# Kernel optimization log

Hardware: AMD Instinct MI355X
Metric: run time of the kernel (lower is better)

Reference implementation:

```python
import jax, jax.numpy as jnp
import numpy as np

D_HEAD = 64  # per-head dim 'd' from init_kwargs


def layer_norm(x, g, b, eps=1e-5):
    m = x.mean(-1, keepdims=True)
    v = x.var(-1, keepdims=True)  # biased var, matches torch LayerNorm
    return (x - m) / jnp.sqrt(v + eps) * g + b


def setup_inputs() -> dict:
    key = jax.random.key(0)
    ks = jax.random.split(key, 16)
    F = 512
    B, T, N = 2, 8, 1024
    s = 1.0 / np.sqrt(F)
    u = lambda k, shape: jax.random.uniform(k, shape, jnp.float32, -s, s)
    return {
        "x": jax.random.normal(ks[0], (B, T, N, F), jnp.float32),
        "Wq": u(ks[1], (F, F)), "bq": u(ks[2], (F,)),
        "Wk": u(ks[3], (F, F)), "bk": u(ks[4], (F,)),
        "Wv": u(ks[5], (F, F)), "bv": u(ks[6], (F,)),
        "ln_g": jnp.ones((F,), jnp.float32), "ln_b": jnp.zeros((F,), jnp.float32),
        "W1": u(ks[7], (F, F)), "b1": u(ks[8], (F,)),
        "W2": u(ks[9], (F, F)), "b2": u(ks[10], (F,)),
        "lnff_g": jnp.ones((F,), jnp.float32), "lnff_b": jnp.zeros((F,), jnp.float32),
    }


def reference(x, Wq, bq, Wk, bk, Wv, bv, ln_g, ln_b, W1, b1, W2, b2, lnff_g, lnff_b):
    B, T, N, F = x.shape
    h = F // D_HEAD
    # q/k/v projections
    q = x @ Wq + bq
    k = x @ Wk + bk
    v = x @ Wv + bv
    # split last dim into heads (split+cat(dim=0) in torch == head axis here)
    qh = q.reshape(B, T, N, h, D_HEAD)
    kh = k.reshape(B, T, N, h, D_HEAD)
    vh = v.reshape(B, T, N, h, D_HEAD)
    # attention over node axis N per (batch, time, head)
    A = jnp.einsum('btqhd,btkhd->bthqk', qh, kh) / jnp.sqrt(jnp.asarray(D_HEAD, x.dtype))
    A = jax.nn.softmax(A, axis=-1)
    o = jnp.einsum('bthqk,btkhd->btqhd', A, vh).reshape(B, T, N, F)
    # residual + LN
    val = layer_norm(o + x, ln_g, ln_b)
    # FFN + final LN
    ff = jax.nn.relu(val @ W1 + b1) @ W2 + b2
    return layer_norm(ff, lnff_g, lnff_b)
```

## Files before the change

kernel.cpp:

```cpp
#include <hip/hip_runtime.h>
#include <hip/hip_bf16.h>

using bf16 = __hip_bfloat16;
typedef unsigned int u32x4 __attribute__((ext_vector_type(4)));
typedef float f32x4 __attribute__((ext_vector_type(4)));
typedef __bf16 bf16x8 __attribute__((ext_vector_type(8)));

#define DEVI __device__ __forceinline__

DEVI f32x4 mfma16(u32x4 a, u32x4 b, f32x4 c) {
    return __builtin_amdgcn_mfma_f32_16x16x32_bf16(
        __builtin_bit_cast(bf16x8, a), __builtin_bit_cast(bf16x8, b), c, 0, 0, 0);
}

struct bf8 { bf16 h[8]; };

DEVI u32x4 pack8(f32x4 lo, f32x4 hi) {
    bf8 t;
#pragma unroll
    for (int i = 0; i < 4; i++) {
        t.h[i] = __float2bfloat16(lo[i]);
        t.h[4 + i] = __float2bfloat16(hi[i]);
    }
    return __builtin_bit_cast(u32x4, t);
}

DEVI unsigned long long pk4(float a, float b, float c, float d) {
    union { unsigned long long u; bf16 h[4]; } t;
    t.h[0] = __float2bfloat16(a); t.h[1] = __float2bfloat16(b);
    t.h[2] = __float2bfloat16(c); t.h[3] = __float2bfloat16(d);
    return t.u;
}

DEVI unsigned trunc2(float a, float b) {
    return __builtin_amdgcn_perm(__builtin_bit_cast(unsigned, b),
                                 __builtin_bit_cast(unsigned, a), 0x07060302);
}

__global__ __launch_bounds__(256) void prep(
    const float* __restrict__ Wq, const float* __restrict__ Wk,
    const float* __restrict__ Wv, const float* __restrict__ W1,
    const float* __restrict__ W2, const float* __restrict__ x,
    bf16* __restrict__ WT, bf16* __restrict__ xb)
{
    int b = blockIdx.x;
    if (b < 5120) {
        int w = b >> 10;
        const float* src = (w == 0) ? Wq : (w == 1) ? Wk : (w == 2) ? Wv : (w == 3) ? W1 : W2;
        int idx = (b & 1023) * 256 + threadIdx.x;
        int n = idx >> 9, kk = idx & 511;
        WT[(size_t)w * 262144 + idx] = __float2bfloat16(src[kk * 512 + n]);
    } else {
        size_t i = ((size_t)(b - 5120) * 256 + threadIdx.x) * 8;
        f32x4 lo = *(const f32x4*)&x[i];
        f32x4 hi = *(const f32x4*)&x[i + 4];
        *(u32x4*)&xb[i] = pack8(lo, hi);
    }
}

#define GEMM_BODY(EPILOGUE)                                                          \
    constexpr int SP = 72;                                                           \
    __shared__ __align__(16) bf16 As[128 * SP];                                      \
    __shared__ __align__(16) bf16 Bs[128 * SP];                                      \
    const int tid = threadIdx.x;                                                     \
    const int lane = tid & 63, wave = tid >> 6;                                      \
    const int wm = (wave >> 1) * 64, wn = (wave & 1) * 64;                           \
    const int lm = lane & 15, lq = lane >> 4;                                        \
    const int sr = tid >> 3, sc = (tid & 7) * 8;             \
    const bf16* Ap = A + (size_t)(bm + sr) * 512 + sc;                               \
    const bf16* Bp = Bt + (size_t)(bn + sr) * 512 + sc;                              \
    f32x4 acc[4][4];                                                                 \
    _Pragma("unroll") for (int i = 0; i < 4; i++)                                    \
        _Pragma("unroll") for (int j = 0; j < 4; j++)                                \
            acc[i][j] = (f32x4){0.f, 0.f, 0.f, 0.f};                                 \
    u32x4 ar[4], br[4];                                                              \
    _Pragma("unroll") for (int p = 0; p < 4; p++) {                                  \
        ar[p] = *(const u32x4*)(Ap + (size_t)p * 32 * 512);                          \
        br[p] = *(const u32x4*)(Bp + (size_t)p * 32 * 512);                          \
    }                                                                                \
    for (int k0 = 0; k0 < 512; k0 += 64) {                                           \
        __syncthreads();                                                             \
        _Pragma("unroll") for (int p = 0; p < 4; p++) {                              \
            *(u32x4*)&As[(p * 32 + sr) * SP + sc] = ar[p];                           \
            *(u32x4*)&Bs[(p * 32 + sr) * SP + sc] = br[p];                           \
        }                                                                            \
        __syncthreads();                                                             \
        if (k0 < 448) {      \
            _Pragma("unroll") for (int p = 0; p < 4; p++) {                          \
                ar[p] = *(const u32x4*)(Ap + (size_t)p * 32 * 512 + k0 + 64);        \
                br[p] = *(const u32x4*)(Bp + (size_t)p * 32 * 512 + k0 + 64);        \
            }                                                                        \
        }                                                                            \
        _Pragma("unroll") for (int h = 0; h < 2; h++) {                              \
            u32x4 af[4], bfr[4];                                                     \
            _Pragma("unroll") for (int i = 0; i < 4; i++)                            \
                af[i] = *(const u32x4*)&As[(wm + i * 16 + lm) * SP + h * 32 + lq * 8]; \
            _Pragma("unroll") for (int j = 0; j < 4; j++)                            \
                bfr[j] = *(const u32x4*)&Bs[(wn + j * 16 + lm) * SP + h * 32 + lq * 8]; \
            EPILOGUE##_MMA                                                           \
        }                                                                            \
    }

#define SWAPPED_MMA                                                                  \
    _Pragma("unroll") for (int i = 0; i < 4; i++)                                    \
        _Pragma("unroll") for (int j = 0; j < 4; j++)                                \
            acc[i][j] = mfma16(bfr[j], af[i], acc[i][j]);
#define NORMAL_MMA                                                                   \
    _Pragma("unroll") for (int i = 0; i < 4; i++)                                    \
        _Pragma("unroll") for (int j = 0; j < 4; j++)                                \
            acc[i][j] = mfma16(af[i], bfr[j], acc[i][j]);

__global__ __launch_bounds__(256) void gemm_qkv(
    const bf16* __restrict__ A, const bf16* __restrict__ WT,
    const float* __restrict__ bqp, const float* __restrict__ bkp, const float* __restrict__ bvp,
    bf16* __restrict__ qb, bf16* __restrict__ kb, bf16* __restrict__ vT)
{
    const int wsel = blockIdx.y >> 2;
    const int bm = blockIdx.x * 128, bn = (blockIdx.y & 3) * 128;
    const bf16* Bt = WT + (size_t)wsel * 262144;
    const float* bias = (wsel == 0) ? bqp : (wsel == 1) ? bkp : bvp;

    if (wsel < 2) {
        GEMM_BODY(SWAPPED)
        const float scale = (wsel == 0) ? 0.18033688f : 1.0f;
        bf16* dst = (wsel == 0) ? qb : kb;
#pragma unroll
        for (int i = 0; i < 4; i++) {
#pragma unroll
            for (int j = 0; j < 4; j++) {
                int row = bm + wm + i * 16 + lm;
                int colb = bn + wn + j * 16 + lq * 4;
                f32x4 b4 = *(const f32x4*)&bias[colb];
                *(unsigned long long*)&dst[(size_t)row * 512 + colb] =
                    pk4((acc[i][j][0] + b4[0]) * scale, (acc[i][j][1] + b4[1]) * scale,
                        (acc[i][j][2] + b4[2]) * scale, (acc[i][j][3] + b4[3]) * scale);
            }
        }
    } else {
        GEMM_BODY(NORMAL)
#pragma unroll
        for (int i = 0; i < 4; i++) {
#pragma unroll
            for (int j = 0; j < 4; j++) {
                int col = bn + wn + j * 16 + lm;
                float bv = bias[col];
                int rowb = bm + wm + i * 16 + lq * 4;
                int btq = rowb >> 10, node = rowb & 1023;
                int u = node & 31;
                int nodeP = (node & ~31) | (((u >> 2) & 3) << 3) | (((u >> 4) & 1) << 2);
                *(unsigned long long*)&vT[((size_t)((btq * 8 + (col >> 6)) * 64 + (col & 63))) * 1024 + nodeP] =
                    pk4(acc[i][j][0] + bv, acc[i][j][1] + bv,
                        acc[i][j][2] + bv, acc[i][j][3] + bv);
            }
        }
    }
}

template <bool RELU>
__global__ __launch_bounds__(256) void gemm_bt(
    const bf16* __restrict__ A, const bf16* __restrict__ Bt,
    const float* __restrict__ bias, bf16* __restrict__ C)
{
    const int bm = blockIdx.x * 128, bn = blockIdx.y * 128;
    GEMM_BODY(SWAPPED)
#pragma unroll
    for (int i = 0; i < 4; i++) {
#pragma unroll
        for (int j = 0; j < 4; j++) {
            int row = bm + wm + i * 16 + lm;
            int colb = bn + wn + j * 16 + lq * 4;
            f32x4 b4 = *(const f32x4*)&bias[colb];
            float c0 = acc[i][j][0] + b4[0], c1 = acc[i][j][1] + b4[1];
            float c2 = acc[i][j][2] + b4[2], c3 = acc[i][j][3] + b4[3];
            if (RELU) {
                c0 = fmaxf(c0, 0.f); c1 = fmaxf(c1, 0.f);
                c2 = fmaxf(c2, 0.f); c3 = fmaxf(c3, 0.f);
            }
            *(unsigned long long*)&C[(size_t)row * 512 + colb] = pk4(c0, c1, c2, c3);
        }
    }
}

__global__ __launch_bounds__(256, 4) void attn_kernel(
    const bf16* __restrict__ q, const bf16* __restrict__ k,
    const bf16* __restrict__ vT, float* __restrict__ o)
{
    constexpr int KP = 72;
    constexpr int VP = 72;
    __shared__ __align__(16) bf16 Ks[64 * KP];
    __shared__ __align__(16) bf16 Vs[64 * VP];

    const int tid = threadIdx.x, lane = tid & 63, wave = tid >> 6;
    const int group = blockIdx.x;
    const int bt = group >> 3, hh = group & 7;
    const int lm = lane & 15, lq = lane >> 4;
    const int qrow0 = bt * 1024 + blockIdx.y * 128 + wave * 32;

    u32x4 qf[2][2];
#pragma unroll
    for (int tm = 0; tm < 2; tm++)
#pragma unroll
        for (int kk2 = 0; kk2 < 2; kk2++)
            qf[tm][kk2] = *(const u32x4*)&q[(size_t)(qrow0 + tm * 16 + lm) * 512 + hh * 64 + kk2 * 32 + lq * 8];

    const bf16* kbase = k + (size_t)(bt * 1024) * 512 + hh * 64;
    const bf16* vbase = vT + (size_t)group * 64 * 1024;

    const int r0 = tid >> 3, e0 = (tid & 7) * 8;
    const int r1 = (256 + tid) >> 3, e1 = e0;

    f32x4 accO[4][2];
#pragma unroll
    for (int md = 0; md < 4; md++)
#pragma unroll
        for (int tm = 0; tm < 2; tm++) accO[md][tm] = (f32x4){0.f, 0.f, 0.f, 0.f};
    float part[2] = {0.f, 0.f};

    u32x4 kreg0 = *(const u32x4*)&kbase[(size_t)r0 * 512 + e0];
    u32x4 kreg1 = *(const u32x4*)&kbase[(size_t)r1 * 512 + e1];
    u32x4 vreg0 = *(const u32x4*)&vbase[(size_t)r0 * 1024 + e0];
    u32x4 vreg1 = *(const u32x4*)&vbase[(size_t)r1 * 1024 + e1];

    for (int kt = 0; kt < 16; kt++) {
        __syncthreads();
        *(u32x4*)&Ks[r0 * KP + e0] = kreg0;
        *(u32x4*)&Ks[r1 * KP + e1] = kreg1;
        *(u32x4*)&Vs[r0 * VP + e0] = vreg0;
        *(u32x4*)&Vs[r1 * VP + e1] = vreg1;
        __syncthreads();
        if (kt < 15) {
            const bf16* kn = kbase + (size_t)((kt + 1) * 64) * 512;
            const bf16* vn = vbase + (kt + 1) * 64;
            kreg0 = *(const u32x4*)&kn[(size_t)r0 * 512 + e0];
            kreg1 = *(const u32x4*)&kn[(size_t)r1 * 512 + e1];
            vreg0 = *(const u32x4*)&vn[(size_t)r0 * 1024 + e0];
            vreg1 = *(const u32x4*)&vn[(size_t)r1 * 1024 + e1];
        }

#pragma unroll
        for (int kc = 0; kc < 2; kc++) {
            const int t0 = kc * 2;
            u32x4 kf00 = *(const u32x4*)&Ks[(t0 * 16 + lm) * KP + lq * 8];
            u32x4 kf01 = *(const u32x4*)&Ks[(t0 * 16 + lm) * KP + 32 + lq * 8];
            u32x4 kf10 = *(const u32x4*)&Ks[((t0 + 1) * 16 + lm) * KP + lq * 8];
            u32x4 kf11 = *(const u32x4*)&Ks[((t0 + 1) * 16 + lm) * KP + 32 + lq * 8];
            u32x4 pw[2];
#pragma unroll
            for (int tm = 0; tm < 2; tm++) {
                f32x4 s0 = (f32x4){0.f, 0.f, 0.f, 0.f};
                s0 = mfma16(kf00, qf[tm][0], s0);
                s0 = mfma16(kf01, qf[tm][1], s0);
                f32x4 s1 = (f32x4){0.f, 0.f, 0.f, 0.f};
                s1 = mfma16(kf10, qf[tm][0], s1);
                s1 = mfma16(kf11, qf[tm][1], s1);
                float p0 = __builtin_amdgcn_exp2f(s0[0]);
                float p1 = __builtin_amdgcn_exp2f(s0[1]);
                float p2 = __builtin_amdgcn_exp2f(s0[2]);
                float p3 = __builtin_amdgcn_exp2f(s0[3]);
                float p4 = __builtin_amdgcn_exp2f(s1[0]);
                float p5 = __builtin_amdgcn_exp2f(s1[1]);
                float p6 = __builtin_amdgcn_exp2f(s1[2]);
                float p7 = __builtin_amdgcn_exp2f(s1[3]);
                part[tm] += ((p0 + p1) + (p2 + p3)) + ((p4 + p5) + (p6 + p7));
                pw[tm] = (u32x4){trunc2(p0, p1), trunc2(p2, p3),
                                 trunc2(p4, p5), trunc2(p6, p7)};
            }
#pragma unroll
            for (int md = 0; md < 4; md++) {
                u32x4 vf = *(const u32x4*)&Vs[(md * 16 + lm) * VP + kc * 32 + lq * 8];
                accO[md][0] = mfma16(vf, pw[0], accO[md][0]);
                accO[md][1] = mfma16(vf, pw[1], accO[md][1]);
            }
        }
    }

#pragma unroll
    for (int tm = 0; tm < 2; tm++) {
        part[tm] += __shfl_xor(part[tm], 16);
        part[tm] += __shfl_xor(part[tm], 32);
        float linv = 1.0f / part[tm];
#pragma unroll
        for (int md = 0; md < 4; md++) {
            f32x4 r;
#pragma unroll
            for (int i = 0; i < 4; i++) r[i] = accO[md][tm][i] * linv;
            *(f32x4*)&o[(size_t)(qrow0 + tm * 16 + lm) * 512 + hh * 64 + md * 16 + lq * 4] = r;
        }
    }
}

template <bool AF32, bool RES, bool OF32>
__global__ __launch_bounds__(256) void ln_kernel(
    const void* __restrict__ a, const float* __restrict__ res,
    const float* __restrict__ g, const float* __restrict__ bb, void* __restrict__ out)
{
    int row = blockIdx.x * 4 + (threadIdx.x >> 6);
    int lane = threadIdx.x & 63;
    size_t base = (size_t)row * 512 + lane * 8;
    int cbase = lane * 8;

    float x8[8];
    if (AF32) {
        const float* af = (const float*)a;
        f32x4 lo = *(const f32x4*)&af[base];
        f32x4 hi = *(const f32x4*)&af[base + 4];
#pragma unroll
        for (int i = 0; i < 4; i++) { x8[i] = lo[i]; x8[4 + i] = hi[i]; }
    } else {
        bf8 av = __builtin_bit_cast(bf8, *(const u32x4*)&((const bf16*)a)[base]);
#pragma unroll
        for (int i = 0; i < 8; i++) x8[i] = __bfloat162float(av.h[i]);
    }
    if (RES) {
        f32x4 lo = *(const f32x4*)&res[base];
        f32x4 hi = *(const f32x4*)&res[base + 4];
#pragma unroll
        for (int i = 0; i < 4; i++) { x8[i] += lo[i]; x8[4 + i] += hi[i]; }
    }

    float s = 0.f, s2 = 0.f;
#pragma unroll
    for (int i = 0; i < 8; i++) { s += x8[i]; s2 += x8[i] * x8[i]; }
#pragma unroll
    for (int off = 1; off < 64; off <<= 1) {
        s += __shfl_xor(s, off);
        s2 += __shfl_xor(s2, off);
    }
    float mean = s * (1.f / 512.f);
    float var = s2 * (1.f / 512.f) - mean * mean;
    float rstd = rsqrtf(var + 1e-5f);

    f32x4 g0 = *(const f32x4*)&g[cbase], g1 = *(const f32x4*)&g[cbase + 4];
    f32x4 b0 = *(const f32x4*)&bb[cbase], b1v = *(const f32x4*)&bb[cbase + 4];
    float y[8];
#pragma unroll
    for (int i = 0; i < 4; i++) {
        y[i] = (x8[i] - mean) * rstd * g0[i] + b0[i];
        y[4 + i] = (x8[4 + i] - mean) * rstd * g1[i] + b1v[i];
    }
    if (OF32) {
        float* op = (float*)out;
        *(f32x4*)&op[base] = (f32x4){y[0], y[1], y[2], y[3]};
        *(f32x4*)&op[base + 4] = (f32x4){y[4], y[5], y[6], y[7]};
    } else {
        bf8 ov;
#pragma unroll
        for (int i = 0; i < 8; i++) ov.h[i] = __float2bfloat16(y[i]);
        *(u32x4*)&((bf16*)out)[base] = __builtin_bit_cast(u32x4, ov);
    }
}

extern "C" void kernel_launch(void* const* d_in, const int* in_sizes, int n_in,
                              void* d_out, int out_size, void* d_ws, size_t ws_size,
                              hipStream_t stream)
{
    const float* x    = (const float*)d_in[0];
    const float* Wq   = (const float*)d_in[1];
    const float* bq   = (const float*)d_in[2];
    const float* Wk   = (const float*)d_in[3];
    const float* bk   = (const float*)d_in[4];
    const float* Wv   = (const float*)d_in[5];
    const float* bv   = (const float*)d_in[6];
    const float* ln_g = (const float*)d_in[7];
    const float* ln_b = (const float*)d_in[8];
    const float* W1   = (const float*)d_in[9];
    const float* b1   = (const float*)d_in[10];
    const float* W2   = (const float*)d_in[11];
    const float* b2   = (const float*)d_in[12];
    const float* lnffg = (const float*)d_in[13];
    const float* lnffb = (const float*)d_in[14];
    float* out = (float*)d_out;

    bf16* ws = (bf16*)d_ws;
    bf16* WT = ws;
    bf16* qb = ws + 5 * 262144;
    bf16* kb = qb + 8388608;
    bf16* vT = kb + 8388608;
    bf16* vl = qb;
    bf16* f1 = kb;
    bf16* f2 = vT;
    bf16* xb = (bf16*)d_out;

    prep<<<9216, 256, 0, stream>>>(Wq, Wk, Wv, W1, W2, x, WT, xb);

    gemm_qkv<<<dim3(128, 12), 256, 0, stream>>>(xb, WT, bq, bk, bv, qb, kb, vT);

    attn_kernel<<<dim3(128, 8), 256, 0, stream>>>(qb, kb, vT, out);

    ln_kernel<true, true, false><<<4096, 256, 0, stream>>>(out, x, ln_g, ln_b, vl);

    dim3 gg(128, 4);
    gemm_bt<true> <<<gg, 256, 0, stream>>>(vl, WT + 3 * 262144, b1, f1);
    gemm_bt<false><<<gg, 256, 0, stream>>>(f1, WT + 4 * 262144, b2, f2);

    ln_kernel<false, false, true><<<4096, 256, 0, stream>>>(f2, nullptr, lnffg, lnffb, out);
}
```

Before: 251.3 us.

## Double-buffer attention K/V tiles, compute softmax row sums via MFMA, raise priority

The attention kernel now double-buffers its K and V tiles in shared memory, which removes one of the two barriers per key tile. Softmax denominators are now built by an extra MFMA against a ones-fragment over the bf16-truncated probabilities, replacing per-lane scalar float adds. The PV MFMA block is wrapped in s_setprio to favour matrix issue. The trade-offs are doubled LDS use, which may limit occupancy, and denominators that now come from the truncated bf16 values instead of fp32, which could shift numerics slightly.

```diff
diff --git a/kernel.cpp b/kernel.cpp
--- a/kernel.cpp
+++ b/kernel.cpp
@@ -187,8 +187,8 @@
 {
     constexpr int KP = 72;
     constexpr int VP = 72;
-    __shared__ __align__(16) bf16 Ks[64 * KP];
-    __shared__ __align__(16) bf16 Vs[64 * VP];
+    __shared__ __align__(16) bf16 Ks[2][64 * KP];
+    __shared__ __align__(16) bf16 Vs[2][64 * VP];
 
     const int tid = threadIdx.x, lane = tid & 63, wave = tid >> 6;
     const int group = blockIdx.x;
@@ -207,43 +207,47 @@
     const bf16* vbase = vT + (size_t)group * 64 * 1024;
 
     const int r0 = tid >> 3, e0 = (tid & 7) * 8;
-    const int r1 = (256 + tid) >> 3, e1 = e0;
+    const int r1 = (256 + tid) >> 3;
+
+    const unsigned ow = (lm == 0) ? 0x3F803F80u : 0u;
+    const u32x4 onesA = (u32x4){ow, ow, ow, ow};
 
     f32x4 accO[4][2];
 #pragma unroll
     for (int md = 0; md < 4; md++)
 #pragma unroll
         for (int tm = 0; tm < 2; tm++) accO[md][tm] = (f32x4){0.f, 0.f, 0.f, 0.f};
-    float part[2] = {0.f, 0.f};
+    f32x4 accL[2] = {(f32x4){0.f, 0.f, 0.f, 0.f}, (f32x4){0.f, 0.f, 0.f, 0.f}};
 
     u32x4 kreg0 = *(const u32x4*)&kbase[(size_t)r0 * 512 + e0];
-    u32x4 kreg1 = *(const u32x4*)&kbase[(size_t)r1 * 512 + e1];
+    u32x4 kreg1 = *(const u32x4*)&kbase[(size_t)r1 * 512 + e0];
     u32x4 vreg0 = *(const u32x4*)&vbase[(size_t)r0 * 1024 + e0];
-    u32x4 vreg1 = *(const u32x4*)&vbase[(size_t)r1 * 1024 + e1];
+    u32x4 vreg1 = *(const u32x4*)&vbase[(size_t)r1 * 1024 + e0];
 
     for (int kt = 0; kt < 16; kt++) {
-        __syncthreads();
-        *(u32x4*)&Ks[r0 * KP + e0] = kreg0;
-        *(u32x4*)&Ks[r1 * KP + e1] = kreg1;
-        *(u32x4*)&Vs[r0 * VP + e0] = vreg0;
-        *(u32x4*)&Vs[r1 * VP + e1] = vreg1;
+        bf16* Kb = Ks[kt & 1];
+        bf16* Vb = Vs[kt & 1];
+        *(u32x4*)&Kb[r0 * KP + e0] = kreg0;
+        *(u32x4*)&Kb[r1 * KP + e0] = kreg1;
+        *(u32x4*)&Vb[r0 * VP + e0] = vreg0;
+        *(u32x4*)&Vb[r1 * VP + e0] = vreg1;
         __syncthreads();
         if (kt < 15) {
             const bf16* kn = kbase + (size_t)((kt + 1) * 64) * 512;
             const bf16* vn = vbase + (kt + 1) * 64;
             kreg0 = *(const u32x4*)&kn[(size_t)r0 * 512 + e0];
-            kreg1 = *(const u32x4*)&kn[(size_t)r1 * 512 + e1];
+            kreg1 = *(const u32x4*)&kn[(size_t)r1 * 512 + e0];
             vreg0 = *(const u32x4*)&vn[(size_t)r0 * 1024 + e0];
-            vreg1 = *(const u32x4*)&vn[(size_t)r1 * 1024 + e1];
+            vreg1 = *(const u32x4*)&vn[(size_t)r1 * 1024 + e0];
         }
 
 #pragma unroll
         for (int kc = 0; kc < 2; kc++) {
             const int t0 = kc * 2;
-            u32x4 kf00 = *(const u32x4*)&Ks[(t0 * 16 + lm) * KP + lq * 8];
-            u32x4 kf01 = *(const u32x4*)&Ks[(t0 * 16 + lm) * KP + 32 + lq * 8];
-            u32x4 kf10 = *(const u32x4*)&Ks[((t0 + 1) * 16 + lm) * KP + lq * 8];
-            u32x4 kf11 = *(const u32x4*)&Ks[((t0 + 1) * 16 + lm) * KP + 32 + lq * 8];
+            u32x4 kf00 = *(const u32x4*)&Kb[(t0 * 16 + lm) * KP + lq * 8];
+            u32x4 kf01 = *(const u32x4*)&Kb[(t0 * 16 + lm) * KP + 32 + lq * 8];
+            u32x4 kf10 = *(const u32x4*)&Kb[((t0 + 1) * 16 + lm) * KP + lq * 8];
+            u32x4 kf11 = *(const u32x4*)&Kb[((t0 + 1) * 16 + lm) * KP + 32 + lq * 8];
             u32x4 pw[2];
 #pragma unroll
             for (int tm = 0; tm < 2; tm++) {
@@ -261,24 +265,28 @@
                 float p5 = __builtin_amdgcn_exp2f(s1[1]);
                 float p6 = __builtin_amdgcn_exp2f(s1[2]);
                 float p7 = __builtin_amdgcn_exp2f(s1[3]);
-                part[tm] += ((p0 + p1) + (p2 + p3)) + ((p4 + p5) + (p6 + p7));
                 pw[tm] = (u32x4){trunc2(p0, p1), trunc2(p2, p3),
                                  trunc2(p4, p5), trunc2(p6, p7)};
             }
+            accL[0] = mfma16(onesA, pw[0], accL[0]);
+            accL[1] = mfma16(onesA, pw[1], accL[1]);
+            __builtin_amdgcn_s_setprio(1);
 #pragma unroll
             for (int md = 0; md < 4; md++) {
-                u32x4 vf = *(const u32x4*)&Vs[(md * 16 + lm) * VP + kc * 32 + lq * 8];
+                u32x4 vf = *(const u32x4*)&Vb[(md * 16 + lm) * VP + kc * 32 + lq * 8];
                 accO[md][0] = mfma16(vf, pw[0], accO[md][0]);
                 accO[md][1] = mfma16(vf, pw[1], accO[md][1]);
             }
+            __builtin_amdgcn_s_setprio(0);
         }
     }
 
 #pragma unroll
     for (int tm = 0; tm < 2; tm++) {
-        part[tm] += __shfl_xor(part[tm], 16);
-        part[tm] += __shfl_xor(part[tm], 32);
-        float linv = 1.0f / part[tm];
+        float l = accL[tm][0];
+        l += __shfl_xor(l, 16);
+        l += __shfl_xor(l, 32);
+        float linv = 1.0f / l;
 #pragma unroll
         for (int md = 0; md < 4; md++) {
             f32x4 r;
```

Result: faster. 243.9 us (-2.9%).
